# Optimization experiments

Measured on AMD Instinct MI355X. Metric: run time of the kernel, lower is better.

## Reference

```python
import jax, jax.numpy as jnp
import numpy as np


def _grid_pull_linear_zero(input, grid):
    """Trilinear grid_pull, bound='zero', extrapolate=False, prefilter=False.
    input: (B, C, Nx, Ny, Nz); grid: (B, 3, Xo, Yo, Zo) voxel coords.
    """
    g = jnp.moveaxis(grid, 1, -1)                      # (B, Xo, Yo, Zo, 3)
    B, C, Nx, Ny, Nz = input.shape
    sizes = jnp.array([Nx, Ny, Nz], dtype=jnp.int32)
    f = jnp.floor(g)
    w = g - f                                          # fractional part in [0,1)
    f = f.astype(jnp.int32)
    inp_flat = input.reshape(B, C, -1)                 # (B, C, Nx*Ny*Nz)
    out = jnp.zeros((B, C, g.shape[1] * g.shape[2] * g.shape[3]), input.dtype)
    for dx in (0, 1):
        for dy in (0, 1):
            for dz in (0, 1):
                off = jnp.array([dx, dy, dz], dtype=jnp.int32)
                idx = f + off                          # (B,Xo,Yo,Zo,3)
                # zero bound: out-of-range taps contribute nothing
                valid = jnp.all((idx >= 0) & (idx < sizes), axis=-1)
                wc = jnp.prod(jnp.where(off == 1, w, 1.0 - w), axis=-1)
                ic = jnp.clip(idx, 0, sizes - 1)
                flat = (ic[..., 0] * Ny + ic[..., 1]) * Nz + ic[..., 2]
                vals = jnp.take_along_axis(inp_flat, flat.reshape(B, 1, -1), axis=2)
                out = out + vals * (wc * valid).reshape(B, 1, -1).astype(input.dtype)
    out = out.reshape(B, C, g.shape[1], g.shape[2], g.shape[3])
    # extrapolate=False: zero voxels sampled outside the field of view
    inb = jnp.all((g >= 0) & (g <= (sizes - 1).astype(g.dtype)), axis=-1)
    return out * inb[:, None].astype(out.dtype)


def setup_inputs() -> dict:
    key = jax.random.key(0)
    k1, k2 = jax.random.split(key)
    B, C, N = 2, 2, 128
    input = jax.random.normal(k1, (B, C, N, N, N), dtype=jnp.float32)
    # voxel coordinates spanning the full input volume [0, N-1]
    grid = jax.random.uniform(k2, (B, 3, N, N, N), dtype=jnp.float32) * (N - 1)
    return {"input": input, "grid": grid}


def reference(input, grid):
    return _grid_pull_linear_zero(input, grid)
```

## Files before the change

kernel.cpp:

```cpp
#include <hip/hip_runtime.h>


#define NDIM  128
#define NV    (128 * 128 * 128)
#define NPTS  (2 * NV)
#define NSLAB 8
#define CAP   270336
#define NBLKB 2048

typedef float f4 __attribute__((ext_vector_type(4)));
typedef float f2 __attribute__((ext_vector_type(2)));
typedef int   i4 __attribute__((ext_vector_type(4)));

__global__ void p0_zero(int* __restrict__ cursor) {
    if (threadIdx.x < NSLAB) cursor[threadIdx.x] = 0;
}

__global__ __launch_bounds__(256) void p2_repack(
    const float* __restrict__ inb,
    float* __restrict__ pk)
{
    const int t  = blockIdx.x * blockDim.x + threadIdx.x;
    const int v  = t << 2;
    const f4 a = *reinterpret_cast<const f4*>(inb + v);
    const f4 c = *reinterpret_cast<const f4*>(inb + NV + v);
    f4 w0, w1;
    w0.x = a.x; w0.y = c.x; w0.z = a.y; w0.w = c.y;
    w1.x = a.z; w1.y = c.z; w1.z = a.w; w1.w = c.w;
    float* o = pk + 2 * v;
    *reinterpret_cast<f4*>(o)     = w0;
    *reinterpret_cast<f4*>(o + 4) = w1;
}

__global__ __launch_bounds__(256) void p3_scatter(
    const float* __restrict__ gb,
    f4* __restrict__ rec,
    int* __restrict__ pos,
    int* __restrict__ cursor)
{
    __shared__ int lcnt[NSLAB];
    __shared__ int lbase[NSLAB];
    const int t = blockIdx.x * blockDim.x + threadIdx.x;
    const int s = t << 2;

    if (threadIdx.x < NSLAB) lcnt[threadIdx.x] = 0;
    __syncthreads();

    const f4 gx = __builtin_nontemporal_load(reinterpret_cast<const f4*>(gb + s));
    const f4 gy = __builtin_nontemporal_load(reinterpret_cast<const f4*>(gb + NV + s));
    const f4 gz = __builtin_nontemporal_load(reinterpret_cast<const f4*>(gb + 2 * NV + s));

    int mybin[4], myrank[4];
#pragma unroll
    for (int k = 0; k < 4; ++k) {
        const int ix = (int)floorf(gx[k]);
        mybin[k]  = min(max(ix, 0), NDIM - 1) >> 4;
        myrank[k] = atomicAdd(&lcnt[mybin[k]], 1);
    }
    __syncthreads();
    if (threadIdx.x < NSLAB)
        lbase[threadIdx.x] = atomicAdd(&cursor[threadIdx.x], lcnt[threadIdx.x]);
    __syncthreads();

    i4 dvec;
#pragma unroll
    for (int k = 0; k < 4; ++k) {
        const int d = mybin[k] * CAP + lbase[mybin[k]] + myrank[k];
        f4 r;
        r.x = gx[k]; r.y = gy[k]; r.z = gz[k];
        r.w = __int_as_float(s + k);
        __builtin_nontemporal_store(r, &rec[d]);
        dvec[k] = d;
    }
    __builtin_nontemporal_store(dvec, reinterpret_cast<i4*>(pos + s));
}

__global__ __launch_bounds__(256) void p4_gather(
    const float* __restrict__ pk,
    const f4* __restrict__ rec,
    f2* __restrict__ res,
    const int* __restrict__ cursor)
{
    const int bin   = blockIdx.x & 7;
    const int chunk = blockIdx.x >> 3;
    const int cnt   = cursor[bin];
    const int seg   = bin * CAP;

    for (int i = chunk * 1024 + (threadIdx.x << 2); i < cnt; i += 256 * 1024) {
        bool live[4];
        f4 r[4];
#pragma unroll
        for (int k = 0; k < 4; ++k) {
            live[k] = (i + k) < cnt;
            r[k] = rec[live[k] ? (seg + i + k) : seg];
        }
        f4 t00[4], t01[4], t10[4], t11[4];
        bool inb[4], interior[4];
        float wx[4], wy[4], wz[4];
        int ixa[4], iya[4], iza[4];
#pragma unroll
        for (int k = 0; k < 4; ++k) {
            const float x = r[k].x, y = r[k].y, z = r[k].z;
            const float fx = floorf(x), fy = floorf(y), fz = floorf(z);
            wx[k] = x - fx; wy[k] = y - fy; wz[k] = z - fz;
            const int ix = (int)fx, iy = (int)fy, iz = (int)fz;
            ixa[k] = ix; iya[k] = iy; iza[k] = iz;
            inb[k] = (x >= 0.0f) & (x <= (float)(NDIM - 1)) &
                     (y >= 0.0f) & (y <= (float)(NDIM - 1)) &
                     (z >= 0.0f) & (z <= (float)(NDIM - 1));
            interior[k] = inb[k] &
                          ((unsigned)ix < (unsigned)(NDIM - 1)) &
                          ((unsigned)iy < (unsigned)(NDIM - 1)) &
                          ((unsigned)iz < (unsigned)(NDIM - 1));
            const int base = interior[k] ? ((ix << 14) + (iy << 7) + iz) : 0;
            const f4* q = reinterpret_cast<const f4*>(pk + 2 * base);
            t00[k] = q[0];
            t01[k] = q[64];
            t10[k] = q[8192];
            t11[k] = q[8256];
        }
#pragma unroll
        for (int k = 0; k < 4; ++k) {
            float acc0 = 0.0f, acc1 = 0.0f;
            const float wz0 = 1.0f - wz[k];
            if (interior[k]) {
                const float wx0 = 1.0f - wx[k], wy0 = 1.0f - wy[k];
                const float w00 = wx0 * wy0,  w01 = wx0 * wy[k];
                const float w10 = wx[k] * wy0, w11 = wx[k] * wy[k];
                const float z00a = fmaf(t00[k].z, wz[k], t00[k].x * wz0);
                const float z01a = fmaf(t01[k].z, wz[k], t01[k].x * wz0);
                const float z10a = fmaf(t10[k].z, wz[k], t10[k].x * wz0);
                const float z11a = fmaf(t11[k].z, wz[k], t11[k].x * wz0);
                acc0 = fmaf(z11a, w11, fmaf(z10a, w10, fmaf(z01a, w01, z00a * w00)));
                const float z00b = fmaf(t00[k].w, wz[k], t00[k].y * wz0);
                const float z01b = fmaf(t01[k].w, wz[k], t01[k].y * wz0);
                const float z10b = fmaf(t10[k].w, wz[k], t10[k].y * wz0);
                const float z11b = fmaf(t11[k].w, wz[k], t11[k].y * wz0);
                acc1 = fmaf(z11b, w11, fmaf(z10b, w10, fmaf(z01b, w01, z00b * w00)));
            } else if (inb[k]) {
                for (int dx = 0; dx < 2; ++dx) {
                    const int X = ixa[k] + dx;
                    if ((unsigned)X >= (unsigned)NDIM) continue;
                    const float wxd = dx ? wx[k] : 1.0f - wx[k];
                    for (int dy = 0; dy < 2; ++dy) {
                        const int Y = iya[k] + dy;
                        if ((unsigned)Y >= (unsigned)NDIM) continue;
                        const float wyd = dy ? wy[k] : 1.0f - wy[k];
                        for (int dz = 0; dz < 2; ++dz) {
                            const int Z = iza[k] + dz;
                            if ((unsigned)Z >= (unsigned)NDIM) continue;
                            const float w = wxd * wyd * (dz ? wz[k] : wz0);
                            const f2 v = *reinterpret_cast<const f2*>(
                                pk + 2 * ((X << 14) + (Y << 7) + Z));
                            acc0 = fmaf(v.x, w, acc0);
                            acc1 = fmaf(v.y, w, acc1);
                        }
                    }
                }
            }
            if (live[k]) {
                f2 o; o.x = acc0; o.y = acc1;
                res[seg + i + k] = o;
            }
        }
    }
}

__global__ __launch_bounds__(256) void p5_unpermute(
    const f2* __restrict__ res,
    const int* __restrict__ pos,
    float* __restrict__ outb)
{
    const int t = blockIdx.x * blockDim.x + threadIdx.x;
    const int s = t << 2;
    const i4 dd = __builtin_nontemporal_load(reinterpret_cast<const i4*>(pos + s));
    const f2 r0 = res[dd.x];
    const f2 r1 = res[dd.y];
    const f2 r2 = res[dd.z];
    const f2 r3 = res[dd.w];
    f4 o0, o1;
    o0.x = r0.x; o0.y = r1.x; o0.z = r2.x; o0.w = r3.x;
    o1.x = r0.y; o1.y = r1.y; o1.z = r2.y; o1.w = r3.y;
    __builtin_nontemporal_store(o0, reinterpret_cast<f4*>(outb + s));
    __builtin_nontemporal_store(o1, reinterpret_cast<f4*>(outb + NV + s));
}

__global__ __launch_bounds__(256) void grid_pull_packed_kernel(
    const float* __restrict__ pk,
    const float* __restrict__ grid,
    float* __restrict__ out)
{
    const int t  = blockIdx.x * blockDim.x + threadIdx.x;
    const int p4i = t << 2;
    const int b  = p4i >> 21;
    const int s  = p4i & (NV - 1);
    const float* gbase = grid + (size_t)b * 3 * NV;
    const f4 gx = *reinterpret_cast<const f4*>(gbase + s);
    const f4 gy = *reinterpret_cast<const f4*>(gbase + NV + s);
    const f4 gz = *reinterpret_cast<const f4*>(gbase + 2 * NV + s);
    const float* p = pk + (size_t)b * 2 * NV;
    f4 o0, o1;
#pragma unroll
    for (int k = 0; k < 4; ++k) {
        const float x = gx[k], y = gy[k], z = gz[k];
        const float fx = floorf(x), fy = floorf(y), fz = floorf(z);
        const float wx = x - fx, wy = y - fy, wz = z - fz;
        const int ix = (int)fx, iy = (int)fy, iz = (int)fz;
        const bool inb = (x >= 0.0f) & (x <= (float)(NDIM - 1)) &
                         (y >= 0.0f) & (y <= (float)(NDIM - 1)) &
                         (z >= 0.0f) & (z <= (float)(NDIM - 1));
        float acc0 = 0.0f, acc1 = 0.0f;
        if (inb) {
            for (int dx = 0; dx < 2; ++dx) {
                const int X = ix + dx;
                if ((unsigned)X >= (unsigned)NDIM) continue;
                const float wxd = dx ? wx : 1.0f - wx;
                for (int dy = 0; dy < 2; ++dy) {
                    const int Y = iy + dy;
                    if ((unsigned)Y >= (unsigned)NDIM) continue;
                    const float wyd = dy ? wy : 1.0f - wy;
                    for (int dz = 0; dz < 2; ++dz) {
                        const int Z = iz + dz;
                        if ((unsigned)Z >= (unsigned)NDIM) continue;
                        const float w = wxd * wyd * (dz ? wz : 1.0f - wz);
                        const f2 v = *reinterpret_cast<const f2*>(
                            p + (X << 15) + (Y << 8) + (Z << 1));
                        acc0 = fmaf(v.x, w, acc0);
                        acc1 = fmaf(v.y, w, acc1);
                    }
                }
            }
        }
        o0[k] = acc0; o1[k] = acc1;
    }
    float* obase = out + (size_t)b * 2 * NV + s;
    *reinterpret_cast<f4*>(obase)      = o0;
    *reinterpret_cast<f4*>(obase + NV) = o1;
}

__global__ __launch_bounds__(256) void grid_pull_direct_kernel(
    const float* __restrict__ input,
    const float* __restrict__ grid,
    float* __restrict__ out)
{
    const int t  = blockIdx.x * blockDim.x + threadIdx.x;
    const int p4i = t << 2;
    const int b  = p4i >> 21;
    const int s  = p4i & (NV - 1);
    const float* gbase = grid + (size_t)b * 3 * NV;
    const f4 gx = *reinterpret_cast<const f4*>(gbase + s);
    const f4 gy = *reinterpret_cast<const f4*>(gbase + NV + s);
    const f4 gz = *reinterpret_cast<const f4*>(gbase + 2 * NV + s);
    const float* in0 = input + (size_t)b * 2 * NV;
    const float* in1 = in0 + NV;
    f4 o0, o1;
#pragma unroll
    for (int k = 0; k < 4; ++k) {
        const float x = gx[k], y = gy[k], z = gz[k];
        const float fx = floorf(x), fy = floorf(y), fz = floorf(z);
        const float wx = x - fx, wy = y - fy, wz = z - fz;
        const int ix = (int)fx, iy = (int)fy, iz = (int)fz;
        const bool inb = (x >= 0.0f) & (x <= (float)(NDIM - 1)) &
                         (y >= 0.0f) & (y <= (float)(NDIM - 1)) &
                         (z >= 0.0f) & (z <= (float)(NDIM - 1));
        float acc0 = 0.0f, acc1 = 0.0f;
        if (inb) {
            for (int dx = 0; dx < 2; ++dx) {
                const int X = ix + dx;
                if ((unsigned)X >= (unsigned)NDIM) continue;
                const float wxd = dx ? wx : 1.0f - wx;
                for (int dy = 0; dy < 2; ++dy) {
                    const int Y = iy + dy;
                    if ((unsigned)Y >= (unsigned)NDIM) continue;
                    const float wyd = dy ? wy : 1.0f - wy;
                    for (int dz = 0; dz < 2; ++dz) {
                        const int Z = iz + dz;
                        if ((unsigned)Z >= (unsigned)NDIM) continue;
                        const float w = wxd * wyd * (dz ? wz : 1.0f - wz);
                        const int idx = (X << 14) + (Y << 7) + Z;
                        acc0 = fmaf(in0[idx], w, acc0);
                        acc1 = fmaf(in1[idx], w, acc1);
                    }
                }
            }
        }
        o0[k] = acc0; o1[k] = acc1;
    }
    float* obase = out + (size_t)b * 2 * NV + s;
    *reinterpret_cast<f4*>(obase)      = o0;
    *reinterpret_cast<f4*>(obase + NV) = o1;
}

extern "C" void kernel_launch(void* const* d_in, const int* in_sizes, int n_in,
                              void* d_out, int out_size, void* d_ws, size_t ws_size,
                              hipStream_t stream) {
    const float* input = (const float*)d_in[0];
    const float* grid  = (const float*)d_in[1];
    float* out         = (float*)d_out;

    const size_t rec_bytes = (size_t)NSLAB * CAP * sizeof(f4);
    const size_t res_bytes = (size_t)NSLAB * CAP * sizeof(f2);
    const size_t pk_bytes  = (size_t)2 * NV * sizeof(float);
    const size_t pos_bytes = (size_t)NV * sizeof(int);
    const size_t need_bin  = rec_bytes + res_bytes + pk_bytes + pos_bytes + 256;
    const size_t need_pack = (size_t)2 * 2 * NV * sizeof(float);

    const int block = 256;

    if (ws_size >= need_bin) {
        char* w = (char*)d_ws;
        f4*   rec    = (f4*)w;
        f2*   res    = (f2*)(w + rec_bytes);
        float* pk    = (float*)(w + rec_bytes + res_bytes);
        int*  pos    = (int*)(w + rec_bytes + res_bytes + pk_bytes);
        int*  cursor = (int*)(w + rec_bytes + res_bytes + pk_bytes + pos_bytes);

        for (int b = 0; b < 2; ++b) {
            const float* inb = input + (size_t)b * 2 * NV;
            const float* gb  = grid  + (size_t)b * 3 * NV;
            float* outb      = out   + (size_t)b * 2 * NV;
            p0_zero<<<1, 64, 0, stream>>>(cursor);
            p2_repack<<<NBLKB, block, 0, stream>>>(inb, pk);
            p3_scatter<<<NBLKB, block, 0, stream>>>(gb, rec, pos, cursor);
            p4_gather<<<NBLKB, block, 0, stream>>>(pk, rec, res, cursor);
            p5_unpermute<<<NBLKB, block, 0, stream>>>(res, pos, outb);
        }
    } else if (ws_size >= need_pack) {
        float* pk = (float*)d_ws;
        for (int b = 0; b < 2; ++b)
            p2_repack<<<NBLKB, block, 0, stream>>>(input + (size_t)b * 2 * NV,
                                                   pk + (size_t)b * 2 * NV);
        grid_pull_packed_kernel<<<2 * NBLKB, block, 0, stream>>>(pk, grid, out);
    } else {
        grid_pull_direct_kernel<<<2 * NBLKB, block, 0, stream>>>(input, grid, out);
    }
}
```

Before: 298.4 us.

## Merge batches into one binned pass and scatter results directly to output

Both batch items now go through a single set of launches, with 16 bins (8 x-slabs per batch) instead of a per-batch loop. The gather kernel writes each result straight to its original output position, using the index stored in the record. This removes the unpermute kernel and the intermediate result and position buffers, along with their memory traffic and launch overhead. In exchange the output writes become scattered scalar stores rather than coalesced vector stores, and the workspace needs twice as many bin records.

Measured after the change: 422.2 us. +41.5%, slower.

```diff
diff --git a/kernel.cpp b/kernel.cpp
--- a/kernel.cpp
+++ b/kernel.cpp
@@ -4,87 +4,91 @@
 #define NDIM  128
 #define NV    (128 * 128 * 128)
 #define NPTS  (2 * NV)
-#define NSLAB 8
+#define NBINS 16
 #define CAP   270336
-#define NBLKB 2048
+#define NBLK  4096
 
 typedef float f4 __attribute__((ext_vector_type(4)));
 typedef float f2 __attribute__((ext_vector_type(2)));
-typedef int   i4 __attribute__((ext_vector_type(4)));
 
 __global__ void p0_zero(int* __restrict__ cursor) {
-    if (threadIdx.x < NSLAB) cursor[threadIdx.x] = 0;
+    if (threadIdx.x < NBINS) cursor[threadIdx.x] = 0;
 }
 
 __global__ __launch_bounds__(256) void p2_repack(
-    const float* __restrict__ inb,
-    float* __restrict__ pk)
+    const float* __restrict__ input, float* __restrict__ pk)
 {
     const int t  = blockIdx.x * blockDim.x + threadIdx.x;
-    const int v  = t << 2;
-    const f4 a = *reinterpret_cast<const f4*>(inb + v);
-    const f4 c = *reinterpret_cast<const f4*>(inb + NV + v);
+    const int v4 = t << 2;
+    const int b  = v4 >> 21;
+    const int v  = v4 & (NV - 1);
+    const float* base = input + (size_t)b * 2 * NV;
+    const f4 a = __builtin_nontemporal_load(reinterpret_cast<const f4*>(base + v));
+    const f4 c = __builtin_nontemporal_load(reinterpret_cast<const f4*>(base + NV + v));
     f4 w0, w1;
     w0.x = a.x; w0.y = c.x; w0.z = a.y; w0.w = c.y;
     w1.x = a.z; w1.y = c.z; w1.z = a.w; w1.w = c.w;
-    float* o = pk + 2 * v;
+    float* o = pk + (size_t)b * 2 * NV + 2 * v;
     *reinterpret_cast<f4*>(o)     = w0;
     *reinterpret_cast<f4*>(o + 4) = w1;
 }
 
 __global__ __launch_bounds__(256) void p3_scatter(
-    const float* __restrict__ gb,
+    const float* __restrict__ grid,
     f4* __restrict__ rec,
-    int* __restrict__ pos,
     int* __restrict__ cursor)
 {
-    __shared__ int lcnt[NSLAB];
-    __shared__ int lbase[NSLAB];
-    const int t = blockIdx.x * blockDim.x + threadIdx.x;
-    const int s = t << 2;
-
-    if (threadIdx.x < NSLAB) lcnt[threadIdx.x] = 0;
+    __shared__ int lcnt[NBINS];
+    __shared__ int lbase[NBINS];
+    const int t  = blockIdx.x * blockDim.x + threadIdx.x;
+    const int s4 = t << 2;
+    const int b  = s4 >> 21;
+    const int s  = s4 & (NV - 1);
+
+    if (threadIdx.x < NBINS) lcnt[threadIdx.x] = 0;
     __syncthreads();
 
-    const f4 gx = __builtin_nontemporal_load(reinterpret_cast<const f4*>(gb + s));
-    const f4 gy = __builtin_nontemporal_load(reinterpret_cast<const f4*>(gb + NV + s));
-    const f4 gz = __builtin_nontemporal_load(reinterpret_cast<const f4*>(gb + 2 * NV + s));
+    const float* gbase = grid + (size_t)b * 3 * NV;
+    const f4 gx = __builtin_nontemporal_load(reinterpret_cast<const f4*>(gbase + s));
+    const f4 gy = __builtin_nontemporal_load(reinterpret_cast<const f4*>(gbase + NV + s));
+    const f4 gz = __builtin_nontemporal_load(reinterpret_cast<const f4*>(gbase + 2 * NV + s));
 
     int mybin[4], myrank[4];
 #pragma unroll
     for (int k = 0; k < 4; ++k) {
         const int ix = (int)floorf(gx[k]);
-        mybin[k]  = min(max(ix, 0), NDIM - 1) >> 4;
+        mybin[k]  = (b << 3) + (min(max(ix, 0), NDIM - 1) >> 4);
         myrank[k] = atomicAdd(&lcnt[mybin[k]], 1);
     }
     __syncthreads();
-    if (threadIdx.x < NSLAB)
+    if (threadIdx.x < NBINS)
         lbase[threadIdx.x] = atomicAdd(&cursor[threadIdx.x], lcnt[threadIdx.x]);
     __syncthreads();
 
-    i4 dvec;
 #pragma unroll
     for (int k = 0; k < 4; ++k) {
         const int d = mybin[k] * CAP + lbase[mybin[k]] + myrank[k];
         f4 r;
         r.x = gx[k]; r.y = gy[k]; r.z = gz[k];
-        r.w = __int_as_float(s + k);
+        r.w = __int_as_float(s4 + k);
         __builtin_nontemporal_store(r, &rec[d]);
-        dvec[k] = d;
-    }
-    __builtin_nontemporal_store(dvec, reinterpret_cast<i4*>(pos + s));
+    }
 }
 
 __global__ __launch_bounds__(256) void p4_gather(
     const float* __restrict__ pk,
     const f4* __restrict__ rec,
-    f2* __restrict__ res,
-    const int* __restrict__ cursor)
-{
-    const int bin   = blockIdx.x & 7;
-    const int chunk = blockIdx.x >> 3;
+    const int* __restrict__ cursor,
+    float* __restrict__ out)
+{
+    const int bid = blockIdx.x;
+    const int bin   = (bid < (NBLK / 2)) ? (bid & 7) : 8 + (bid & 7);
+    const int chunk = (bid & (NBLK / 2 - 1)) >> 3;
     const int cnt   = cursor[bin];
+    const int b     = bin >> 3;
     const int seg   = bin * CAP;
+    const float* pkb = pk  + (size_t)b * 2 * NV;
+    float* outb      = out + (size_t)b * 2 * NV;
 
     for (int i = chunk * 1024 + (threadIdx.x << 2); i < cnt; i += 256 * 1024) {
         bool live[4];
@@ -113,7 +117,7 @@
                           ((unsigned)iy < (unsigned)(NDIM - 1)) &
                           ((unsigned)iz < (unsigned)(NDIM - 1));
             const int base = interior[k] ? ((ix << 14) + (iy << 7) + iz) : 0;
-            const f4* q = reinterpret_cast<const f4*>(pk + 2 * base);
+            const f4* q = reinterpret_cast<const f4*>(pkb + 2 * base);
             t00[k] = q[0];
             t01[k] = q[64];
             t10[k] = q[8192];
@@ -125,7 +129,7 @@
             const float wz0 = 1.0f - wz[k];
             if (interior[k]) {
                 const float wx0 = 1.0f - wx[k], wy0 = 1.0f - wy[k];
-                const float w00 = wx0 * wy0,  w01 = wx0 * wy[k];
+                const float w00 = wx0 * wy0,   w01 = wx0 * wy[k];
                 const float w10 = wx[k] * wy0, w11 = wx[k] * wy[k];
                 const float z00a = fmaf(t00[k].z, wz[k], t00[k].x * wz0);
                 const float z01a = fmaf(t01[k].z, wz[k], t01[k].x * wz0);
@@ -151,7 +155,7 @@
                             if ((unsigned)Z >= (unsigned)NDIM) continue;
                             const float w = wxd * wyd * (dz ? wz[k] : wz0);
                             const f2 v = *reinterpret_cast<const f2*>(
-                                pk + 2 * ((X << 14) + (Y << 7) + Z));
+                                pkb + 2 * ((X << 14) + (Y << 7) + Z));
                             acc0 = fmaf(v.x, w, acc0);
                             acc1 = fmaf(v.y, w, acc1);
                         }
@@ -159,30 +163,12 @@
                 }
             }
             if (live[k]) {
-                f2 o; o.x = acc0; o.y = acc1;
-                res[seg + i + k] = o;
+                const int sp = __float_as_int(r[k].w) & (NV - 1);
+                __builtin_nontemporal_store(acc0, outb + sp);
+                __builtin_nontemporal_store(acc1, outb + NV + sp);
             }
         }
     }
-}
-
-__global__ __launch_bounds__(256) void p5_unpermute(
-    const f2* __restrict__ res,
-    const int* __restrict__ pos,
-    float* __restrict__ outb)
-{
-    const int t = blockIdx.x * blockDim.x + threadIdx.x;
-    const int s = t << 2;
-    const i4 dd = __builtin_nontemporal_load(reinterpret_cast<const i4*>(pos + s));
-    const f2 r0 = res[dd.x];
-    const f2 r1 = res[dd.y];
-    const f2 r2 = res[dd.z];
-    const f2 r3 = res[dd.w];
-    f4 o0, o1;
-    o0.x = r0.x; o0.y = r1.x; o0.z = r2.x; o0.w = r3.x;
-    o1.x = r0.y; o1.y = r1.y; o1.z = r2.y; o1.w = r3.y;
-    __builtin_nontemporal_store(o0, reinterpret_cast<f4*>(outb + s));
-    __builtin_nontemporal_store(o1, reinterpret_cast<f4*>(outb + NV + s));
 }
 
 __global__ __launch_bounds__(256) void grid_pull_packed_kernel(
@@ -298,40 +284,28 @@
     const float* grid  = (const float*)d_in[1];
     float* out         = (float*)d_out;
 
-    const size_t rec_bytes = (size_t)NSLAB * CAP * sizeof(f4);
-    const size_t res_bytes = (size_t)NSLAB * CAP * sizeof(f2);
-    const size_t pk_bytes  = (size_t)2 * NV * sizeof(float);
-    const size_t pos_bytes = (size_t)NV * sizeof(int);
-    const size_t need_bin  = rec_bytes + res_bytes + pk_bytes + pos_bytes + 256;
-    const size_t need_pack = (size_t)2 * 2 * NV * sizeof(float);
+    const size_t rec_bytes = (size_t)NBINS * CAP * sizeof(f4);
+    const size_t pk_bytes  = (size_t)NPTS * 2 * sizeof(float);
+    const size_t need_bin  = rec_bytes + pk_bytes + 256;
+    const size_t need_pack = pk_bytes;
 
     const int block = 256;
 
     if (ws_size >= need_bin) {
         char* w = (char*)d_ws;
-        f4*   rec    = (f4*)w;
-        f2*   res    = (f2*)(w + rec_bytes);
-        float* pk    = (float*)(w + rec_bytes + res_bytes);
-        int*  pos    = (int*)(w + rec_bytes + res_bytes + pk_bytes);
-        int*  cursor = (int*)(w + rec_bytes + res_bytes + pk_bytes + pos_bytes);
-
-        for (int b = 0; b < 2; ++b) {
-            const float* inb = input + (size_t)b * 2 * NV;
-            const float* gb  = grid  + (size_t)b * 3 * NV;
-            float* outb      = out   + (size_t)b * 2 * NV;
-            p0_zero<<<1, 64, 0, stream>>>(cursor);
-            p2_repack<<<NBLKB, block, 0, stream>>>(inb, pk);
-            p3_scatter<<<NBLKB, block, 0, stream>>>(gb, rec, pos, cursor);
-            p4_gather<<<NBLKB, block, 0, stream>>>(pk, rec, res, cursor);
-            p5_unpermute<<<NBLKB, block, 0, stream>>>(res, pos, outb);
-        }
+        f4*    rec    = (f4*)w;
+        float* pk     = (float*)(w + rec_bytes);
+        int*   cursor = (int*)(w + rec_bytes + pk_bytes);
+
+        p0_zero<<<1, 64, 0, stream>>>(cursor);
+        p2_repack<<<NBLK, block, 0, stream>>>(input, pk);
+        p3_scatter<<<NBLK, block, 0, stream>>>(grid, rec, cursor);
+        p4_gather<<<NBLK, block, 0, stream>>>(pk, rec, cursor, out);
     } else if (ws_size >= need_pack) {
         float* pk = (float*)d_ws;
-        for (int b = 0; b < 2; ++b)
-            p2_repack<<<NBLKB, block, 0, stream>>>(input + (size_t)b * 2 * NV,
-                                                   pk + (size_t)b * 2 * NV);
-        grid_pull_packed_kernel<<<2 * NBLKB, block, 0, stream>>>(pk, grid, out);
+        p2_repack<<<NBLK, block, 0, stream>>>(input, pk);
+        grid_pull_packed_kernel<<<NBLK, block, 0, stream>>>(pk, grid, out);
     } else {
-        grid_pull_direct_kernel<<<2 * NBLKB, block, 0, stream>>>(input, grid, out);
-    }
-}
+        grid_pull_direct_kernel<<<NBLK, block, 0, stream>>>(input, grid, out);
+    }
+}
```
